# Kernel optimization log

Hardware: AMD Instinct MI355X
Metric: run time of the kernel (lower is better)

## Reference

```python
import jax, jax.numpy as jnp
import numpy as np

B, T, UD, YD, ZD, HD, L = 1024, 1024, 16, 16, 16, 128, 2


def setup_inputs() -> dict:
    key = jax.random.key(0)
    ks = iter(jax.random.split(key, 40))
    r = lambda *s: jax.random.normal(next(ks), s, jnp.float32) * 0.05
    inp = dict(
        u=jax.random.normal(next(ks), (B, UD, T), jnp.float32),
        y=jax.random.normal(next(ks), (B, YD, T), jnp.float32),
        h0=jax.random.uniform(next(ks), (L, B, HD), jnp.float32),
        phi_u_w0=r(HD, UD), phi_u_b0=r(HD), phi_u_w1=r(HD, HD), phi_u_b1=r(HD),
        dynn_w0=r(HD, 2 * HD), dynn_b0=r(HD), dynn_w1=r(HD, HD), dynn_b1=r(HD),
        x_mean_w=r(ZD, HD), x_mean_b=r(ZD),
        x_logvar_w=r(ZD, HD), x_logvar_b=r(ZD),
        phi_x_w0=r(HD, 2 * ZD), phi_x_b0=r(HD), phi_x_w1=r(HD, HD), phi_x_b1=r(HD),
        menn_w0=r(HD, HD), menn_b0=r(HD), menn_w1=r(YD, HD), menn_b1=r(YD),
        gru_wih=r(L, 3 * HD, HD), gru_whh=r(L, 3 * HD, HD),
        C=r(YD, ZD),
    )
    return inp


def _mlp2(x, w0, b0, w1, b1):
    # Linear -> ReLU -> Linear (torch Linear: y = x W^T + b)
    return jax.nn.relu(x @ w0.T + b0) @ w1.T + b1


def reference(u, y, h0,
              phi_u_w0, phi_u_b0, phi_u_w1, phi_u_b1,
              dynn_w0, dynn_b0, dynn_w1, dynn_b1,
              x_mean_w, x_mean_b, x_logvar_w, x_logvar_b,
              phi_x_w0, phi_x_b0, phi_x_w1, phi_x_b1,
              menn_w0, menn_b0, menn_w1, menn_b1,
              gru_wih, gru_whh, C):
    uT = jnp.moveaxis(u, 2, 0)  # (T, B, UD)
    yT = jnp.moveaxis(y, 2, 0)  # (T, B, YD)

    def step(h, xy):
        u_t, y_t = xy
        phi_u_t = _mlp2(u_t, phi_u_w0, phi_u_b0, phi_u_w1, phi_u_b1)  # (B, HD)
        dphi = _mlp2(jnp.concatenate([phi_u_t, h[-1]], axis=1),
                     dynn_w0, dynn_b0, dynn_w1, dynn_b1)
        x_mean = dphi @ x_mean_w.T + x_mean_b      # (B, ZD)
        x_logvar = dphi @ x_logvar_w.T + x_logvar_b
        # single-step multi-layer GRU (no bias), PyTorch gate order r,z,n
        x = phi_u_t
        hs = []
        for l in range(L):
            gi = x @ gru_wih[l].T          # (B, 3HD)
            gh = h[l] @ gru_whh[l].T
            ir, iz, inn = jnp.split(gi, 3, axis=1)
            hr, hz, hn = jnp.split(gh, 3, axis=1)
            rg = jax.nn.sigmoid(ir + hr)
            zg = jax.nn.sigmoid(iz + hz)
            ng = jnp.tanh(inn + rg * hn)
            hl = (1.0 - zg) * ng + zg * h[l]
            hs.append(hl)
            x = hl
        h_new = jnp.stack(hs, axis=0)
        # mpnt_wt >= 10 branch: NN measurement + physics measurement C @ x_mean
        phi_x = _mlp2(jnp.concatenate([x_mean, x_logvar], axis=1),
                      phi_x_w0, phi_x_b0, phi_x_w1, phi_x_b1)
        y_hat = _mlp2(phi_x, menn_w0, menn_b0, menn_w1, menn_b1) + x_mean @ C.T
        loss_t = jnp.sum((y_hat - y_t) ** 2)
        return h_new, loss_t

    _, losses = jax.lax.scan(step, h0, (uT, yT))
    return jnp.sum(losses)
```

## Files before the change

### kernel.cpp

```cpp
#include <hip/hip_runtime.h>
#include <hip/hip_bf16.h>

typedef unsigned short u16;
typedef unsigned int u32;
using short8 = __attribute__((ext_vector_type(8))) short;
using f32x4  = __attribute__((ext_vector_type(4))) float;

#define DEVINL static __device__ __forceinline__

DEVINL float bf2f(u16 u){
  union { unsigned int i; float f; } x; x.i = ((unsigned int)u) << 16; return x.f;
}
DEVINL u16 f2bf(float f){
  union { float f; unsigned int i; } x; x.f = f;
  unsigned int i = x.i;
  return (u16)((i + 0x7FFFu + ((i >> 16) & 1u)) >> 16);
}
DEVINL u16 f2bf1(float f){
  __hip_bfloat16 b = __float2bfloat16(f);
  u16 u; __builtin_memcpy(&u, &b, 2); return u;
}
DEVINL float fast_sigm(float x){
  float e = __builtin_amdgcn_exp2f(x * -1.442695041f);
  return __builtin_amdgcn_rcpf(1.f + e);
}
DEVINL float fast_tanh(float x){
  x = fminf(fmaxf(x, -10.f), 10.f);
  float e = __builtin_amdgcn_exp2f(x * -2.885390082f);
  return (1.f - e) * __builtin_amdgcn_rcpf(1.f + e);
}
DEVINL f32x4 zero4(){ f32x4 z = {0.f, 0.f, 0.f, 0.f}; return z; }

DEVINL f32x4 mfma16(short8 a, short8 b, f32x4 c){
  return __builtin_amdgcn_mfma_f32_16x16x32_bf16(a, b, c, 0, 0, 0);
}

DEVINL short8 frag_ld(const u16* base, int stride){
  int l = threadIdx.x & 63;
  return *(const short8*)(base + (l & 15) * stride + ((l >> 4) << 3));
}
DEVINL short8 gfrag(const u16* rowbase, int stride, int ks){
  int l = threadIdx.x & 63;
  return *(const short8*)(rowbase + (size_t)(l & 15) * stride + ks * 32 + ((l >> 4) << 3));
}

DEVINL void acc_store_lds(u16* dst, int stride, int col_base, f32x4 acc, float bias, bool relu){
  int l = threadIdx.x & 63;
  int col = col_base + (l & 15);
  int row0 = (l >> 4) * 4;
  #pragma unroll
  for (int r = 0; r < 4; r++){
    float v = acc[r] + bias;
    if (relu) v = fmaxf(v, 0.f);
    dst[(row0 + r) * stride + col] = f2bf(v);
  }
}

DEVINL void stage_weights(u16* dst, const float* src, int N, int K, int Kp){
  int stride = Kp + 8;
  if (Kp > K){
    int padw = Kp - K;
    for (int i = threadIdx.x; i < N * padw; i += blockDim.x){
      int n = i / padw, k = K + (i - (i / padw) * padw);
      dst[n * stride + k] = 0;
    }
  }
  for (int i = threadIdx.x * 4; i < N * K; i += blockDim.x * 4){
    float4 v = *(const float4*)(src + i);
    int n = i / K, k = i - n * K;
    u16* d = dst + n * stride + k;
    d[0] = f2bf(v.x); d[1] = f2bf(v.y); d[2] = f2bf(v.z); d[3] = f2bf(v.w);
  }
}

__global__ __launch_bounds__(256) void k_inith(const float* __restrict__ h0, u16* __restrict__ hst){
  int i = blockIdx.x * 256 + threadIdx.x;
  if (i < 2 * 1024 * 128) hst[i] = f2bf(h0[i]);
}

__global__ __launch_bounds__(512, 4) void k_phiu(const float* __restrict__ u,
    const float* __restrict__ w0, const float* __restrict__ b0,
    const float* __restrict__ w1, const float* __restrict__ b1,
    u16* __restrict__ phi, int t0, int Tc){
  __shared__ __align__(16) u16 w0s[128 * 40];
  __shared__ __align__(16) u16 w1s[128 * 136];
  __shared__ __align__(16) u16 buf[8][16 * 136];
  stage_weights(w0s, w0, 128, 16, 32);
  stage_weights(w1s, w1, 128, 128, 128);
  int wv = threadIdx.x >> 6, l = threadIdx.x & 63;
  u16* mybuf = buf[wv];
  float b0v[8], b1v[8];
  #pragma unroll
  for (int nt = 0; nt < 8; nt++){
    b0v[nt] = b0[nt * 16 + (l & 15)];
    b1v[nt] = b1[nt * 16 + (l & 15)];
  }
  __syncthreads();
  int tpb = Tc >> 4;
  int ntile = 1024 * tpb;
  int stride = gridDim.x * 8;
  for (int tile = blockIdx.x * 8 + wv; tile < ntile; tile += stride){
    int b = tile / tpb;
    int tt = (tile - b * tpb) << 4;
    int t = l & 15, kb = l >> 4;
    #pragma unroll
    for (int j = 0; j < 4; j++){
      int k = kb + j * 4;
      mybuf[t * 136 + k] = f2bf(u[(size_t)(b * 16 + k) * 1024 + t0 + tt + t]);
      mybuf[t * 136 + 16 + k] = 0;
    }
    short8 a0 = frag_ld(mybuf, 136);
    f32x4 acc[8];
    #pragma unroll
    for (int nt = 0; nt < 8; nt++)
      acc[nt] = mfma16(a0, frag_ld(w0s + nt * 16 * 40, 40), zero4());
    #pragma unroll
    for (int nt = 0; nt < 8; nt++)
      acc_store_lds(mybuf, 136, nt * 16, acc[nt], b0v[nt], true);
    f32x4 a2[8];
    #pragma unroll
    for (int nt = 0; nt < 8; nt++) a2[nt] = zero4();
    #pragma unroll
    for (int ks = 0; ks < 4; ks++){
      short8 a = frag_ld(mybuf + ks * 32, 136);
      #pragma unroll
      for (int nt = 0; nt < 8; nt++)
        a2[nt] = mfma16(a, frag_ld(w1s + nt * 16 * 136 + ks * 32, 136), a2[nt]);
    }
    #pragma unroll
    for (int nt = 0; nt < 8; nt++)
      acc_store_lds(mybuf, 136, nt * 16, a2[nt], b1v[nt], false);
    u16* dst = phi + (size_t)(b * Tc + tt) * 128;
    #pragma unroll
    for (int j = 0; j < 4; j++){
      int c = j * 64 + l;
      int row = c >> 4, k = (c & 15) * 8;
      *(short8*)(dst + row * 128 + k) = *(const short8*)(mybuf + row * 136 + k);
    }
  }
}

__global__ __launch_bounds__(256, 1) void k_gru(const u16* __restrict__ phi,
    const float* __restrict__ gwih, const float* __restrict__ gwhh,
    u16* __restrict__ hst, u16* __restrict__ Hs, int Tc){
  __shared__ __align__(16) u16 wi0[384 * 136];
  __shared__ __align__(16) u16 h0s[2][16 * 136];
  __shared__ __align__(16) u16 h1s[2][16 * 136];
  __shared__ __align__(16) u16 pb[4][16 * 136];
  const int l = threadIdx.x & 63;
  const int wv = threadIdx.x >> 6;
  const int b0 = blockIdx.x * 16;
  const int m0 = (l >> 4) * 4;
  const int cc = l & 15;
  const int nb = wv * 32;

  stage_weights(wi0, gwih, 384, 128, 128);

  const float* srcs[3] = { gwhh, gwih + 49152, gwhh + 49152 };
  short8 Wr[3][3][2][4];
  #pragma unroll
  for (int mm = 0; mm < 3; mm++){
    #pragma unroll
    for (int g = 0; g < 3; g++){
      #pragma unroll
      for (int nt = 0; nt < 2; nt++){
        int n = g * 128 + nb + nt * 16 + cc;
        #pragma unroll
        for (int ks = 0; ks < 4; ks++){
          const float* p = srcs[mm] + (size_t)n * 128 + ks * 32 + ((l >> 4) << 3);
          float4 va = *(const float4*)p;
          float4 vb = *(const float4*)(p + 4);
          short8 f;
          f[0] = (short)f2bf(va.x); f[1] = (short)f2bf(va.y);
          f[2] = (short)f2bf(va.z); f[3] = (short)f2bf(va.w);
          f[4] = (short)f2bf(vb.x); f[5] = (short)f2bf(vb.y);
          f[6] = (short)f2bf(vb.z); f[7] = (short)f2bf(vb.w);
          Wr[mm][g][nt][ks] = f;
        }
      }
    }
  }
  const int row = threadIdx.x >> 4, k0 = (threadIdx.x & 15) * 8;
  *(uint4*)(&h0s[0][row * 136 + k0]) = *(const uint4*)(hst + (size_t)(b0 + row) * 128 + k0);
  *(uint4*)(&h1s[0][row * 136 + k0]) = *(const uint4*)(hst + 131072 + (size_t)(b0 + row) * 128 + k0);
  float hp0[2][4], hp1[2][4];
  #pragma unroll
  for (int nt = 0; nt < 2; nt++)
    #pragma unroll
    for (int r = 0; r < 4; r++){
      hp0[nt][r] = bf2f(hst[(size_t)(b0 + m0 + r) * 128 + nb + nt * 16 + cc]);
      hp1[nt][r] = bf2f(hst[131072 + (size_t)(b0 + m0 + r) * 128 + nb + nt * 16 + cc]);
    }
  const u16* pL = phi + (size_t)(b0 + row) * Tc * 128 + k0;
  u16* Hp = Hs + (size_t)(b0 + row) * Tc * 128 + k0;
  *(uint4*)(&pb[0][row * 136 + k0]) = *(const uint4*)(pL);
  *(uint4*)(&pb[1][row * 136 + k0]) = *(const uint4*)(pL + 128);
  uint4 pfA = *(const uint4*)(pL + 2 * 128);
  uint4 pfB = *(const uint4*)(pL + 3 * 128);
  __syncthreads();

  auto ITER = [&](int i, int P, int q, uint4& pf){
    short8 a0[4];
    #pragma unroll
    for (int ks = 0; ks < 4; ks++) a0[ks] = frag_ld(h0s[P] + ks * 32, 136);
    if (i > 0){
      short8 a1[4];
      #pragma unroll
      for (int ks = 0; ks < 4; ks++) a1[ks] = frag_ld(h1s[P ^ 1] + ks * 32, 136);
      *(uint4*)(Hp + (size_t)(i - 1) * 128) = *(const uint4*)(&h1s[P ^ 1][row * 136 + k0]);
      f32x4 cr[2], cz[2], cin[2], chn[2];
      #pragma unroll
      for (int nt = 0; nt < 2; nt++){ cr[nt]=zero4(); cz[nt]=zero4(); cin[nt]=zero4(); chn[nt]=zero4(); }
      #pragma unroll
      for (int ks = 0; ks < 4; ks++)
        #pragma unroll
        for (int nt = 0; nt < 2; nt++){
          cr[nt]  = mfma16(a0[ks], Wr[1][0][nt][ks], cr[nt]);
          cr[nt]  = mfma16(a1[ks], Wr[2][0][nt][ks], cr[nt]);
          cz[nt]  = mfma16(a0[ks], Wr[1][1][nt][ks], cz[nt]);
          cz[nt]  = mfma16(a1[ks], Wr[2][1][nt][ks], cz[nt]);
          cin[nt] = mfma16(a0[ks], Wr[1][2][nt][ks], cin[nt]);
          chn[nt] = mfma16(a1[ks], Wr[2][2][nt][ks], chn[nt]);
        }
      #pragma unroll
      for (int nt = 0; nt < 2; nt++)
        #pragma unroll
        for (int r = 0; r < 4; r++){
          float rg = fast_sigm(cr[nt][r]);
          float zg = fast_sigm(cz[nt][r]);
          float ng = fast_tanh(cin[nt][r] + rg * chn[nt][r]);
          float hv = zg * (hp1[nt][r] - ng) + ng;
          hp1[nt][r] = hv;
          h1s[P][(m0 + r) * 136 + nb + nt * 16 + cc] = f2bf1(hv);
        }
    }
    if (i < Tc){
      short8 ap[4];
      #pragma unroll
      for (int ks = 0; ks < 4; ks++) ap[ks] = frag_ld(pb[q] + ks * 32, 136);
      f32x4 cr[2], cz[2], cin[2], chn[2];
      #pragma unroll
      for (int nt = 0; nt < 2; nt++){ cr[nt]=zero4(); cz[nt]=zero4(); cin[nt]=zero4(); chn[nt]=zero4(); }
      #pragma unroll
      for (int ks = 0; ks < 4; ks++)
        #pragma unroll
        for (int nt = 0; nt < 2; nt++){
          cr[nt]  = mfma16(ap[ks], frag_ld(wi0 + (0 * 128 + nb + nt * 16) * 136 + ks * 32, 136), cr[nt]);
          cr[nt]  = mfma16(a0[ks], Wr[0][0][nt][ks], cr[nt]);
          cz[nt]  = mfma16(ap[ks], frag_ld(wi0 + (1 * 128 + nb + nt * 16) * 136 + ks * 32, 136), cz[nt]);
          cz[nt]  = mfma16(a0[ks], Wr[0][1][nt][ks], cz[nt]);
          cin[nt] = mfma16(ap[ks], frag_ld(wi0 + (2 * 128 + nb + nt * 16) * 136 + ks * 32, 136), cin[nt]);
          chn[nt] = mfma16(a0[ks], Wr[0][2][nt][ks], chn[nt]);
        }
      if (i + 2 < Tc) *(uint4*)(&pb[(q + 2) & 3][row * 136 + k0]) = pf;
      if (i + 4 < Tc) pf = *(const uint4*)(pL + (size_t)(i + 4) * 128);
      #pragma unroll
      for (int nt = 0; nt < 2; nt++)
        #pragma unroll
        for (int r = 0; r < 4; r++){
          float rg = fast_sigm(cr[nt][r]);
          float zg = fast_sigm(cz[nt][r]);
          float ng = fast_tanh(cin[nt][r] + rg * chn[nt][r]);
          float hv = zg * (hp0[nt][r] - ng) + ng;
          hp0[nt][r] = hv;
          h0s[P ^ 1][(m0 + r) * 136 + nb + nt * 16 + cc] = f2bf1(hv);
        }
    }
    __builtin_amdgcn_sched_barrier(0);
    asm volatile("s_waitcnt lgkmcnt(0)");
    __builtin_amdgcn_s_barrier();
    __builtin_amdgcn_sched_barrier(0);
  };

  for (int i = 0; i < Tc; i += 4){
    ITER(i + 0, 0, 0, pfA);
    ITER(i + 1, 1, 1, pfB);
    ITER(i + 2, 0, 2, pfA);
    ITER(i + 3, 1, 3, pfB);
  }
  ITER(Tc, 0, 0, pfA);
  *(uint4*)(hst + (size_t)(b0 + row) * 128 + k0) = *(const uint4*)(&h0s[0][row * 136 + k0]);
  *(uint4*)(hst + 131072 + (size_t)(b0 + row) * 128 + k0) = *(const uint4*)(&h1s[0][row * 136 + k0]);
}

__global__ __launch_bounds__(512, 2) void k_c1(const u16* __restrict__ phi, const u16* __restrict__ Hs,
    const float* __restrict__ dw0, const float* __restrict__ db0,
    const float* __restrict__ dw1, const float* __restrict__ db1,
    const float* __restrict__ xmw, const float* __restrict__ xmb,
    const float* __restrict__ xlw, const float* __restrict__ xlb,
    u16* __restrict__ xmlv, int Tc){
  __shared__ __align__(16) u16 w0s[128 * 264];
  __shared__ __align__(16) u16 w1s[128 * 136];
  __shared__ __align__(16) u16 xws[32 * 136];
  __shared__ __align__(16) u16 buf[8][16 * 136];
  stage_weights(w0s, dw0, 128, 256, 256);
  stage_weights(w1s, dw1, 128, 128, 128);
  stage_weights(xws, xmw, 16, 128, 128);
  stage_weights(xws + 16 * 136, xlw, 16, 128, 128);
  int wv = threadIdx.x >> 6, l = threadIdx.x & 63;
  u16* mybuf = buf[wv];
  float b0v[8], b1v[8];
  #pragma unroll
  for (int nt = 0; nt < 8; nt++){
    b0v[nt] = db0[nt * 16 + (l & 15)];
    b1v[nt] = db1[nt * 16 + (l & 15)];
  }
  float bxm = xmb[l & 15], bxl = xlb[l & 15];
  __syncthreads();
  int tpb = Tc >> 4;
  int ntile = 1024 * tpb;
  int stride = gridDim.x * 8;
  for (int tile = blockIdx.x * 8 + wv; tile < ntile; tile += stride){
    int b = tile / tpb;
    int tt = (tile - b * tpb) << 4;
    size_t rbase = (size_t)(b * Tc + tt);
    const u16* ap = phi + rbase * 128;
    const u16* hp = Hs + rbase * 128;
    f32x4 acc[8];
    #pragma unroll
    for (int nt = 0; nt < 8; nt++) acc[nt] = zero4();
    #pragma unroll
    for (int ks = 0; ks < 8; ks++){
      short8 a = (ks < 4) ? gfrag(ap, 128, ks) : gfrag(hp, 128, ks - 4);
      #pragma unroll
      for (int nt = 0; nt < 8; nt++)
        acc[nt] = mfma16(a, frag_ld(w0s + nt * 16 * 264 + ks * 32, 264), acc[nt]);
    }
    #pragma unroll
    for (int nt = 0; nt < 8; nt++)
      acc_store_lds(mybuf, 136, nt * 16, acc[nt], b0v[nt], true);
    f32x4 a2[8];
    #pragma unroll
    for (int nt = 0; nt < 8; nt++) a2[nt] = zero4();
    #pragma unroll
    for (int ks = 0; ks < 4; ks++){
      short8 a = frag_ld(mybuf + ks * 32, 136);
      #pragma unroll
      for (int nt = 0; nt < 8; nt++)
        a2[nt] = mfma16(a, frag_ld(w1s + nt * 16 * 136 + ks * 32, 136), a2[nt]);
    }
    #pragma unroll
    for (int nt = 0; nt < 8; nt++)
      acc_store_lds(mybuf, 136, nt * 16, a2[nt], b1v[nt], false);
    f32x4 am = zero4(), al = zero4();
    #pragma unroll
    for (int ks = 0; ks < 4; ks++){
      short8 a = frag_ld(mybuf + ks * 32, 136);
      am = mfma16(a, frag_ld(xws + ks * 32, 136), am);
      al = mfma16(a, frag_ld(xws + 16 * 136 + ks * 32, 136), al);
    }
    acc_store_lds(mybuf, 136, 0, am, bxm, false);
    acc_store_lds(mybuf, 136, 16, al, bxl, false);
    u16* dst = xmlv + rbase * 32;
    int c = l;
    int row = c >> 2, k = (c & 3) * 8;
    *(short8*)(dst + row * 32 + k) = *(const short8*)(mybuf + row * 136 + k);
  }
}

__global__ __launch_bounds__(512, 2) void k_c2(const u16* __restrict__ xmlv, const float* __restrict__ y,
    const float* __restrict__ pw0, const float* __restrict__ pb0,
    const float* __restrict__ pw1, const float* __restrict__ pb1,
    const float* __restrict__ mw0, const float* __restrict__ mb0,
    const float* __restrict__ mw1, const float* __restrict__ mb1,
    const float* __restrict__ Cw, float* __restrict__ out, int t0, int Tc){
  __shared__ __align__(16) u16 pw0s[128 * 40];
  __shared__ __align__(16) u16 pw1s[128 * 136];
  __shared__ __align__(16) u16 mw0s[128 * 136];
  __shared__ __align__(16) u16 mw1s[16 * 136];
  __shared__ __align__(16) u16 Cs[16 * 40];
  __shared__ __align__(16) u16 buf[8][16 * 136];
  stage_weights(pw0s, pw0, 128, 32, 32);
  stage_weights(pw1s, pw1, 128, 128, 128);
  stage_weights(mw0s, mw0, 128, 128, 128);
  stage_weights(mw1s, mw1, 16, 128, 128);
  stage_weights(Cs, Cw, 16, 16, 32);
  int wv = threadIdx.x >> 6, l = threadIdx.x & 63;
  u16* mybuf = buf[wv];
  float bp0v[8], bp1v[8], bm0v[8];
  #pragma unroll
  for (int nt = 0; nt < 8; nt++){
    bp0v[nt] = pb0[nt * 16 + (l & 15)];
    bp1v[nt] = pb1[nt * 16 + (l & 15)];
    bm0v[nt] = mb0[nt * 16 + (l & 15)];
  }
  float bm1 = mb1[l & 15];
  __syncthreads();
  float lacc = 0.f;
  int tpb = Tc >> 4;
  int ntile = 1024 * tpb;
  int stride = gridDim.x * 8;
  for (int tile = blockIdx.x * 8 + wv; tile < ntile; tile += stride){
    int b = tile / tpb;
    int tt = (tile - b * tpb) << 4;
    size_t rbase = (size_t)(b * Tc + tt);
    const u16* xp = xmlv + rbase * 32;
    short8 a0 = gfrag(xp, 32, 0);
    f32x4 acc[8];
    #pragma unroll
    for (int nt = 0; nt < 8; nt++)
      acc[nt] = mfma16(a0, frag_ld(pw0s + nt * 16 * 40, 40), zero4());
    #pragma unroll
    for (int nt = 0; nt < 8; nt++)
      acc_store_lds(mybuf, 136, nt * 16, acc[nt], bp0v[nt], true);
    f32x4 a2[8];
    #pragma unroll
    for (int nt = 0; nt < 8; nt++) a2[nt] = zero4();
    #pragma unroll
    for (int ks = 0; ks < 4; ks++){
      short8 a = frag_ld(mybuf + ks * 32, 136);
      #pragma unroll
      for (int nt = 0; nt < 8; nt++)
        a2[nt] = mfma16(a, frag_ld(pw1s + nt * 16 * 136 + ks * 32, 136), a2[nt]);
    }
    #pragma unroll
    for (int nt = 0; nt < 8; nt++)
      acc_store_lds(mybuf, 136, nt * 16, a2[nt], bp1v[nt], false);
    f32x4 a3[8];
    #pragma unroll
    for (int nt = 0; nt < 8; nt++) a3[nt] = zero4();
    #pragma unroll
    for (int ks = 0; ks < 4; ks++){
      short8 a = frag_ld(mybuf + ks * 32, 136);
      #pragma unroll
      for (int nt = 0; nt < 8; nt++)
        a3[nt] = mfma16(a, frag_ld(mw0s + nt * 16 * 136 + ks * 32, 136), a3[nt]);
    }
    #pragma unroll
    for (int nt = 0; nt < 8; nt++)
      acc_store_lds(mybuf, 136, nt * 16, a3[nt], bm0v[nt], true);
    f32x4 ay = zero4();
    #pragma unroll
    for (int ks = 0; ks < 4; ks++){
      short8 a = frag_ld(mybuf + ks * 32, 136);
      ay = mfma16(a, frag_ld(mw1s + ks * 32, 136), ay);
    }
    f32x4 ac = mfma16(a0, frag_ld(Cs, 40), zero4());
    #pragma unroll
    for (int r = 0; r < 4; r++){
      float yh = ay[r] + bm1 + ac[r];
      int m = (l >> 4) * 4 + r, j = l & 15;
      float d = yh - y[(size_t)(b * 16 + j) * 1024 + t0 + tt + m];
      lacc += d * d;
    }
  }
  #pragma unroll
  for (int off = 32; off > 0; off >>= 1)
    lacc += __shfl_down(lacc, off);
  if (l == 0) atomicAdd(out, lacc);
}

extern "C" void kernel_launch(void* const* d_in, const int* in_sizes, int n_in,
                              void* d_out, int out_size, void* d_ws, size_t ws_size,
                              hipStream_t stream){
  const float* u    = (const float*)d_in[0];
  const float* y    = (const float*)d_in[1];
  const float* h0   = (const float*)d_in[2];
  const float* puw0 = (const float*)d_in[3];
  const float* pub0 = (const float*)d_in[4];
  const float* puw1 = (const float*)d_in[5];
  const float* pub1 = (const float*)d_in[6];
  const float* dw0  = (const float*)d_in[7];
  const float* db0  = (const float*)d_in[8];
  const float* dw1  = (const float*)d_in[9];
  const float* db1  = (const float*)d_in[10];
  const float* xmw  = (const float*)d_in[11];
  const float* xmb  = (const float*)d_in[12];
  const float* xlw  = (const float*)d_in[13];
  const float* xlb  = (const float*)d_in[14];
  const float* pxw0 = (const float*)d_in[15];
  const float* pxb0 = (const float*)d_in[16];
  const float* pxw1 = (const float*)d_in[17];
  const float* pxb1 = (const float*)d_in[18];
  const float* mw0  = (const float*)d_in[19];
  const float* mb0  = (const float*)d_in[20];
  const float* mw1  = (const float*)d_in[21];
  const float* mb1  = (const float*)d_in[22];
  const float* gwih = (const float*)d_in[23];
  const float* gwhh = (const float*)d_in[24];
  const float* Cw   = (const float*)d_in[25];

  char* w = (char*)d_ws;
  u16* hst = (u16*)w; w += (size_t)2 * 1024 * 128 * 2;
  size_t head = (size_t)2 * 1024 * 128 * 2 + 4096;
  size_t avail = (ws_size > head) ? (ws_size - head) : 0;
  int Tc = 1024;
  while (Tc > 64 && (size_t)1024 * (size_t)Tc * (128 + 128 + 32) * 2 > avail) Tc >>= 1;
  u16* phi  = (u16*)w; w += (size_t)1024 * Tc * 128 * 2;
  u16* Hs   = (u16*)w; w += (size_t)1024 * Tc * 128 * 2;
  u16* xmlv = (u16*)w; w += (size_t)1024 * Tc * 32 * 2;

  hipMemsetAsync(d_out, 0, sizeof(float), stream);
  k_inith<<<1024, 256, 0, stream>>>(h0, hst);
  for (int t0 = 0; t0 < 1024; t0 += Tc){
    k_phiu<<<512, 512, 0, stream>>>(u, puw0, pub0, puw1, pub1, phi, t0, Tc);
    k_gru<<<64, 256, 0, stream>>>(phi, gwih, gwhh, hst, Hs, Tc);
    k_c1<<<256, 512, 0, stream>>>(phi, Hs, dw0, db0, dw1, db1, xmw, xmb, xlw, xlb, xmlv, Tc);
    k_c2<<<256, 512, 0, stream>>>(xmlv, y, pxw0, pxb0, pxw1, pxb1, mw0, mb0, mw1, mb1, Cw,
                                  (float*)d_out, t0, Tc);
  }
}
```

Baseline: 3.407 ms.

## Fuse the four stages into one role-split kernel pipelined over time chunks

Merges phiu, GRU, c1 and c2 into a single kernel whose block ranges take different roles, sharing one dynamic LDS buffer. The time axis is cut into small chunks and software-pipelined across launches: in each launch phiu works on chunk j, GRU on j-1, c1 on j-2 and c2 on j-3. Triple-buffered phi and double-buffered Hs and xmlv buffers make this safe. The goal is to hide the embarrassingly parallel MLP stages behind the serial 64-block GRU recurrence instead of running them back to back. The cost is fewer blocks per non-GRU stage, more launches, and a large LDS footprint per block (about 139 KB), which limits residency to one block per CU.

Result: faster. 3.259 ms (-4.3%).

```diff
diff --git a/kernel.cpp b/kernel.cpp
--- a/kernel.cpp
+++ b/kernel.cpp
@@ -78,17 +78,16 @@
   if (i < 2 * 1024 * 128) hst[i] = f2bf(h0[i]);
 }
 
-__global__ __launch_bounds__(512, 4) void k_phiu(const float* __restrict__ u,
-    const float* __restrict__ w0, const float* __restrict__ b0,
-    const float* __restrict__ w1, const float* __restrict__ b1,
-    u16* __restrict__ phi, int t0, int Tc){
-  __shared__ __align__(16) u16 w0s[128 * 40];
-  __shared__ __align__(16) u16 w1s[128 * 136];
-  __shared__ __align__(16) u16 buf[8][16 * 136];
+
+DEVINL void phiu_body(u16* smem, const float* u, const float* w0, const float* b0,
+                      const float* w1, const float* b1, u16* phiW, int t0, int Tc){
+  u16* w0s = smem;
+  u16* w1s = smem + 5120;
+  u16* buf = smem + 22528;
   stage_weights(w0s, w0, 128, 16, 32);
   stage_weights(w1s, w1, 128, 128, 128);
   int wv = threadIdx.x >> 6, l = threadIdx.x & 63;
-  u16* mybuf = buf[wv];
+  u16* mybuf = buf + wv * 2176;
   float b0v[8], b1v[8];
   #pragma unroll
   for (int nt = 0; nt < 8; nt++){
@@ -98,8 +97,8 @@
   __syncthreads();
   int tpb = Tc >> 4;
   int ntile = 1024 * tpb;
-  int stride = gridDim.x * 8;
-  for (int tile = blockIdx.x * 8 + wv; tile < ntile; tile += stride){
+  int stride = 128 * 4;
+  for (int tile = (blockIdx.x - 64) * 4 + wv; tile < ntile; tile += stride){
     int b = tile / tpb;
     int tt = (tile - b * tpb) << 4;
     int t = l & 15, kb = l >> 4;
@@ -130,7 +129,7 @@
     #pragma unroll
     for (int nt = 0; nt < 8; nt++)
       acc_store_lds(mybuf, 136, nt * 16, a2[nt], b1v[nt], false);
-    u16* dst = phi + (size_t)(b * Tc + tt) * 128;
+    u16* dst = phiW + (size_t)(b * Tc + tt) * 128;
     #pragma unroll
     for (int j = 0; j < 4; j++){
       int c = j * 64 + l;
@@ -140,13 +139,13 @@
   }
 }
 
-__global__ __launch_bounds__(256, 1) void k_gru(const u16* __restrict__ phi,
-    const float* __restrict__ gwih, const float* __restrict__ gwhh,
-    u16* __restrict__ hst, u16* __restrict__ Hs, int Tc){
-  __shared__ __align__(16) u16 wi0[384 * 136];
-  __shared__ __align__(16) u16 h0s[2][16 * 136];
-  __shared__ __align__(16) u16 h1s[2][16 * 136];
-  __shared__ __align__(16) u16 pb[4][16 * 136];
+DEVINL void gru_body(u16* smem, const u16* __restrict__ phi,
+                     const float* gwih, const float* gwhh,
+                     u16* hst, u16* Hs, int Tc){
+  u16* wi0 = smem;
+  u16* h0sA[2] = { smem + 52224, smem + 54400 };
+  u16* h1sA[2] = { smem + 56576, smem + 58752 };
+  u16* pbA[4]  = { smem + 60928, smem + 63104, smem + 65280, smem + 67456 };
   const int l = threadIdx.x & 63;
   const int wv = threadIdx.x >> 6;
   const int b0 = blockIdx.x * 16;
@@ -181,8 +180,8 @@
     }
   }
   const int row = threadIdx.x >> 4, k0 = (threadIdx.x & 15) * 8;
-  *(uint4*)(&h0s[0][row * 136 + k0]) = *(const uint4*)(hst + (size_t)(b0 + row) * 128 + k0);
-  *(uint4*)(&h1s[0][row * 136 + k0]) = *(const uint4*)(hst + 131072 + (size_t)(b0 + row) * 128 + k0);
+  *(uint4*)(&h0sA[0][row * 136 + k0]) = *(const uint4*)(hst + (size_t)(b0 + row) * 128 + k0);
+  *(uint4*)(&h1sA[0][row * 136 + k0]) = *(const uint4*)(hst + 131072 + (size_t)(b0 + row) * 128 + k0);
   float hp0[2][4], hp1[2][4];
   #pragma unroll
   for (int nt = 0; nt < 2; nt++)
@@ -193,8 +192,8 @@
     }
   const u16* pL = phi + (size_t)(b0 + row) * Tc * 128 + k0;
   u16* Hp = Hs + (size_t)(b0 + row) * Tc * 128 + k0;
-  *(uint4*)(&pb[0][row * 136 + k0]) = *(const uint4*)(pL);
-  *(uint4*)(&pb[1][row * 136 + k0]) = *(const uint4*)(pL + 128);
+  *(uint4*)(&pbA[0][row * 136 + k0]) = *(const uint4*)(pL);
+  *(uint4*)(&pbA[1][row * 136 + k0]) = *(const uint4*)(pL + 128);
   uint4 pfA = *(const uint4*)(pL + 2 * 128);
   uint4 pfB = *(const uint4*)(pL + 3 * 128);
   __syncthreads();
@@ -202,12 +201,12 @@
   auto ITER = [&](int i, int P, int q, uint4& pf){
     short8 a0[4];
     #pragma unroll
-    for (int ks = 0; ks < 4; ks++) a0[ks] = frag_ld(h0s[P] + ks * 32, 136);
+    for (int ks = 0; ks < 4; ks++) a0[ks] = frag_ld(h0sA[P] + ks * 32, 136);
     if (i > 0){
       short8 a1[4];
       #pragma unroll
-      for (int ks = 0; ks < 4; ks++) a1[ks] = frag_ld(h1s[P ^ 1] + ks * 32, 136);
-      *(uint4*)(Hp + (size_t)(i - 1) * 128) = *(const uint4*)(&h1s[P ^ 1][row * 136 + k0]);
+      for (int ks = 0; ks < 4; ks++) a1[ks] = frag_ld(h1sA[P ^ 1] + ks * 32, 136);
+      *(uint4*)(Hp + (size_t)(i - 1) * 128) = *(const uint4*)(&h1sA[P ^ 1][row * 136 + k0]);
       f32x4 cr[2], cz[2], cin[2], chn[2];
       #pragma unroll
       for (int nt = 0; nt < 2; nt++){ cr[nt]=zero4(); cz[nt]=zero4(); cin[nt]=zero4(); chn[nt]=zero4(); }
@@ -231,13 +230,13 @@
           float ng = fast_tanh(cin[nt][r] + rg * chn[nt][r]);
           float hv = zg * (hp1[nt][r] - ng) + ng;
           hp1[nt][r] = hv;
-          h1s[P][(m0 + r) * 136 + nb + nt * 16 + cc] = f2bf1(hv);
+          h1sA[P][(m0 + r) * 136 + nb + nt * 16 + cc] = f2bf1(hv);
         }
     }
     if (i < Tc){
       short8 ap[4];
       #pragma unroll
-      for (int ks = 0; ks < 4; ks++) ap[ks] = frag_ld(pb[q] + ks * 32, 136);
+      for (int ks = 0; ks < 4; ks++) ap[ks] = frag_ld(pbA[q] + ks * 32, 136);
       f32x4 cr[2], cz[2], cin[2], chn[2];
       #pragma unroll
       for (int nt = 0; nt < 2; nt++){ cr[nt]=zero4(); cz[nt]=zero4(); cin[nt]=zero4(); chn[nt]=zero4(); }
@@ -252,7 +251,7 @@
           cin[nt] = mfma16(ap[ks], frag_ld(wi0 + (2 * 128 + nb + nt * 16) * 136 + ks * 32, 136), cin[nt]);
           chn[nt] = mfma16(a0[ks], Wr[0][2][nt][ks], chn[nt]);
         }
-      if (i + 2 < Tc) *(uint4*)(&pb[(q + 2) & 3][row * 136 + k0]) = pf;
+      if (i + 2 < Tc) *(uint4*)(&pbA[(q + 2) & 3][row * 136 + k0]) = pf;
       if (i + 4 < Tc) pf = *(const uint4*)(pL + (size_t)(i + 4) * 128);
       #pragma unroll
       for (int nt = 0; nt < 2; nt++)
@@ -263,7 +262,7 @@
           float ng = fast_tanh(cin[nt][r] + rg * chn[nt][r]);
           float hv = zg * (hp0[nt][r] - ng) + ng;
           hp0[nt][r] = hv;
-          h0s[P ^ 1][(m0 + r) * 136 + nb + nt * 16 + cc] = f2bf1(hv);
+          h0sA[P ^ 1][(m0 + r) * 136 + nb + nt * 16 + cc] = f2bf1(hv);
         }
     }
     __builtin_amdgcn_sched_barrier(0);
@@ -279,26 +278,24 @@
     ITER(i + 3, 1, 3, pfB);
   }
   ITER(Tc, 0, 0, pfA);
-  *(uint4*)(hst + (size_t)(b0 + row) * 128 + k0) = *(const uint4*)(&h0s[0][row * 136 + k0]);
-  *(uint4*)(hst + 131072 + (size_t)(b0 + row) * 128 + k0) = *(const uint4*)(&h1s[0][row * 136 + k0]);
-}
-
-__global__ __launch_bounds__(512, 2) void k_c1(const u16* __restrict__ phi, const u16* __restrict__ Hs,
-    const float* __restrict__ dw0, const float* __restrict__ db0,
-    const float* __restrict__ dw1, const float* __restrict__ db1,
-    const float* __restrict__ xmw, const float* __restrict__ xmb,
-    const float* __restrict__ xlw, const float* __restrict__ xlb,
-    u16* __restrict__ xmlv, int Tc){
-  __shared__ __align__(16) u16 w0s[128 * 264];
-  __shared__ __align__(16) u16 w1s[128 * 136];
-  __shared__ __align__(16) u16 xws[32 * 136];
-  __shared__ __align__(16) u16 buf[8][16 * 136];
+  *(uint4*)(hst + (size_t)(b0 + row) * 128 + k0) = *(const uint4*)(&h0sA[0][row * 136 + k0]);
+  *(uint4*)(hst + 131072 + (size_t)(b0 + row) * 128 + k0) = *(const uint4*)(&h1sA[0][row * 136 + k0]);
+}
+
+DEVINL void c1_body(u16* smem, const u16* phiC, const u16* HsC,
+    const float* dw0, const float* db0, const float* dw1, const float* db1,
+    const float* xmw, const float* xmb, const float* xlw, const float* xlb,
+    u16* xmlv, int Tc){
+  u16* w0s = smem;
+  u16* w1s = smem + 33792;
+  u16* xws = smem + 51200;
+  u16* buf = smem + 55552;
   stage_weights(w0s, dw0, 128, 256, 256);
   stage_weights(w1s, dw1, 128, 128, 128);
   stage_weights(xws, xmw, 16, 128, 128);
   stage_weights(xws + 16 * 136, xlw, 16, 128, 128);
   int wv = threadIdx.x >> 6, l = threadIdx.x & 63;
-  u16* mybuf = buf[wv];
+  u16* mybuf = buf + wv * 2176;
   float b0v[8], b1v[8];
   #pragma unroll
   for (int nt = 0; nt < 8; nt++){
@@ -309,13 +306,13 @@
   __syncthreads();
   int tpb = Tc >> 4;
   int ntile = 1024 * tpb;
-  int stride = gridDim.x * 8;
-  for (int tile = blockIdx.x * 8 + wv; tile < ntile; tile += stride){
+  int stride = 128 * 4;
+  for (int tile = (blockIdx.x - 192) * 4 + wv; tile < ntile; tile += stride){
     int b = tile / tpb;
     int tt = (tile - b * tpb) << 4;
     size_t rbase = (size_t)(b * Tc + tt);
-    const u16* ap = phi + rbase * 128;
-    const u16* hp = Hs + rbase * 128;
+    const u16* ap = phiC + rbase * 128;
+    const u16* hp = HsC + rbase * 128;
     f32x4 acc[8];
     #pragma unroll
     for (int nt = 0; nt < 8; nt++) acc[nt] = zero4();
@@ -358,25 +355,23 @@
   }
 }
 
-__global__ __launch_bounds__(512, 2) void k_c2(const u16* __restrict__ xmlv, const float* __restrict__ y,
-    const float* __restrict__ pw0, const float* __restrict__ pb0,
-    const float* __restrict__ pw1, const float* __restrict__ pb1,
-    const float* __restrict__ mw0, const float* __restrict__ mb0,
-    const float* __restrict__ mw1, const float* __restrict__ mb1,
-    const float* __restrict__ Cw, float* __restrict__ out, int t0, int Tc){
-  __shared__ __align__(16) u16 pw0s[128 * 40];
-  __shared__ __align__(16) u16 pw1s[128 * 136];
-  __shared__ __align__(16) u16 mw0s[128 * 136];
-  __shared__ __align__(16) u16 mw1s[16 * 136];
-  __shared__ __align__(16) u16 Cs[16 * 40];
-  __shared__ __align__(16) u16 buf[8][16 * 136];
+DEVINL void c2_body(u16* smem, const u16* xmlv, const float* y,
+    const float* pw0, const float* pb0, const float* pw1, const float* pb1,
+    const float* mw0, const float* mb0, const float* mw1, const float* mb1,
+    const float* Cw, float* out, int t0, int Tc){
+  u16* pw0s = smem;
+  u16* pw1s = smem + 5120;
+  u16* mw0s = smem + 22528;
+  u16* mw1s = smem + 39936;
+  u16* Cs   = smem + 42112;
+  u16* buf  = smem + 42752;
   stage_weights(pw0s, pw0, 128, 32, 32);
   stage_weights(pw1s, pw1, 128, 128, 128);
   stage_weights(mw0s, mw0, 128, 128, 128);
   stage_weights(mw1s, mw1, 16, 128, 128);
   stage_weights(Cs, Cw, 16, 16, 32);
   int wv = threadIdx.x >> 6, l = threadIdx.x & 63;
-  u16* mybuf = buf[wv];
+  u16* mybuf = buf + wv * 2176;
   float bp0v[8], bp1v[8], bm0v[8];
   #pragma unroll
   for (int nt = 0; nt < 8; nt++){
@@ -389,8 +384,8 @@
   float lacc = 0.f;
   int tpb = Tc >> 4;
   int ntile = 1024 * tpb;
-  int stride = gridDim.x * 8;
-  for (int tile = blockIdx.x * 8 + wv; tile < ntile; tile += stride){
+  int stride = 128 * 4;
+  for (int tile = (blockIdx.x - 320) * 4 + wv; tile < ntile; tile += stride){
     int b = tile / tpb;
     int tt = (tile - b * tpb) << 4;
     size_t rbase = (size_t)(b * Tc + tt);
@@ -448,6 +443,30 @@
   for (int off = 32; off > 0; off >>= 1)
     lacc += __shfl_down(lacc, off);
   if (l == 0) atomicAdd(out, lacc);
+}
+
+__global__ __launch_bounds__(256, 1) void k_fused(
+    const float* __restrict__ u, const float* __restrict__ y,
+    const float* puw0, const float* pub0, const float* puw1, const float* pub1,
+    const float* dw0, const float* db0, const float* dw1, const float* db1,
+    const float* xmw, const float* xmb, const float* xlw, const float* xlb,
+    const float* pxw0, const float* pxb0, const float* pxw1, const float* pxb1,
+    const float* mw0, const float* mb0, const float* mw1, const float* mb1,
+    const float* Cw, const float* gwih, const float* gwhh,
+    u16* phiW, const u16* phiG, const u16* phiC,
+    u16* hst, u16* HsW, const u16* HsC,
+    u16* xmW, const u16* xmC,
+    float* out, int t0phiu, int t0c2, int Tc, int flags){
+  __shared__ __align__(16) u16 smem[69632];
+  if (blockIdx.x < 64){
+    if (flags & 2) gru_body(smem, phiG, gwih, gwhh, hst, HsW, Tc);
+  } else if (blockIdx.x < 192){
+    if (flags & 1) phiu_body(smem, u, puw0, pub0, puw1, pub1, phiW, t0phiu, Tc);
+  } else if (blockIdx.x < 320){
+    if (flags & 4) c1_body(smem, phiC, HsC, dw0, db0, dw1, db1, xmw, xmb, xlw, xlb, xmW, Tc);
+  } else {
+    if (flags & 8) c2_body(smem, xmC, y, pxw0, pxb0, pxw1, pxb1, mw0, mb0, mw1, mb1, Cw, out, t0c2, Tc);
+  }
 }
 
 extern "C" void kernel_launch(void* const* d_in, const int* in_sizes, int n_in,
@@ -480,23 +499,43 @@
   const float* gwhh = (const float*)d_in[24];
   const float* Cw   = (const float*)d_in[25];
 
-  char* w = (char*)d_ws;
-  u16* hst = (u16*)w; w += (size_t)2 * 1024 * 128 * 2;
-  size_t head = (size_t)2 * 1024 * 128 * 2 + 4096;
-  size_t avail = (ws_size > head) ? (ws_size - head) : 0;
-  int Tc = 1024;
-  while (Tc > 64 && (size_t)1024 * (size_t)Tc * (128 + 128 + 32) * 2 > avail) Tc >>= 1;
-  u16* phi  = (u16*)w; w += (size_t)1024 * Tc * 128 * 2;
-  u16* Hs   = (u16*)w; w += (size_t)1024 * Tc * 128 * 2;
-  u16* xmlv = (u16*)w; w += (size_t)1024 * Tc * 32 * 2;
+  const size_t hstE = (size_t)2 * 1024 * 128;
+  int Tc = 128;
+  while (Tc > 16){
+    size_t needB = (hstE + (size_t)1024 * Tc * (3 * 128 + 2 * 128 + 2 * 32)) * 2 + 4096;
+    if (needB <= ws_size) break;
+    Tc >>= 1;
+  }
+  int NC = 1024 / Tc;
+  size_t phiSz = (size_t)1024 * Tc * 128;
+  size_t xmSz  = (size_t)1024 * Tc * 32;
+
+  u16* hst  = (u16*)d_ws;
+  u16* phiB = hst + hstE;
+  u16* HsB  = phiB + 3 * phiSz;
+  u16* xmB  = HsB + 2 * phiSz;
 
   hipMemsetAsync(d_out, 0, sizeof(float), stream);
   k_inith<<<1024, 256, 0, stream>>>(h0, hst);
-  for (int t0 = 0; t0 < 1024; t0 += Tc){
-    k_phiu<<<512, 512, 0, stream>>>(u, puw0, pub0, puw1, pub1, phi, t0, Tc);
-    k_gru<<<64, 256, 0, stream>>>(phi, gwih, gwhh, hst, Hs, Tc);
-    k_c1<<<256, 512, 0, stream>>>(phi, Hs, dw0, db0, dw1, db1, xmw, xmb, xlw, xlb, xmlv, Tc);
-    k_c2<<<256, 512, 0, stream>>>(xmlv, y, pxw0, pxb0, pxw1, pxb1, mw0, mb0, mw1, mb1, Cw,
-                                  (float*)d_out, t0, Tc);
-  }
-}
+
+  for (int j = 0; j <= NC + 2; j++){
+    int flags = 0;
+    if (j < NC) flags |= 1;
+    if (j >= 1 && j <= NC) flags |= 2;
+    if (j >= 2 && j <= NC + 1) flags |= 4;
+    if (j >= 3) flags |= 8;
+    int s0 = j % 3, s1 = (j + 2) % 3, s2 = (j + 1) % 3;
+    int hw = (j + 1) & 1, hc = j & 1;
+    int xw = j & 1, xc = (j + 1) & 1;
+    k_fused<<<448, 256, 0, stream>>>(
+        u, y,
+        puw0, pub0, puw1, pub1,
+        dw0, db0, dw1, db1, xmw, xmb, xlw, xlb,
+        pxw0, pxb0, pxw1, pxb1, mw0, mb0, mw1, mb1,
+        Cw, gwih, gwhh,
+        phiB + (size_t)s0 * phiSz, phiB + (size_t)s1 * phiSz, phiB + (size_t)s2 * phiSz,
+        hst, HsB + (size_t)hw * phiSz, HsB + (size_t)hc * phiSz,
+        xmB + (size_t)xw * xmSz, xmB + (size_t)xc * xmSz,
+        (float*)d_out, j * Tc, (j - 3) * Tc, Tc, flags);
+  }
+}
```
